# Kernel tuning notes

Hardware: AMD Instinct MI355X
Metric: run time of the kernel (lower is better)

Reference implementation:

```python
import jax, jax.numpy as jnp
import numpy as np

B, S, DIM = 2, 2048, 4096
H, KV, HD = 32, 8, 128
REP = H // KV
SCALE = HD ** -0.5
ROPE_THETA = 10000.0


def setup_inputs() -> dict:
    key = jax.random.key(0)
    ks = jax.random.split(key, 6)
    x = jax.random.normal(ks[0], (B, S, DIM), dtype=jnp.float32)
    # weights stored [in, out]; y = x @ W matches nn.Linear(in,out,bias=False)
    wq = jax.random.normal(ks[1], (DIM, H * HD), dtype=jnp.float32) * (DIM ** -0.5)
    wk = jax.random.normal(ks[2], (DIM, KV * HD), dtype=jnp.float32) * (DIM ** -0.5)
    wv = jax.random.normal(ks[3], (DIM, KV * HD), dtype=jnp.float32) * (DIM ** -0.5)
    wo = jax.random.normal(ks[4], (H * HD, DIM), dtype=jnp.float32) * ((H * HD) ** -0.5)
    # RoPE tables: angle[t, j] = t * theta^(-2j/hd)
    inv_freq = 1.0 / (ROPE_THETA ** (np.arange(0, HD, 2, dtype=np.float32) / HD))
    t = np.arange(S, dtype=np.float32)
    angles = np.outer(t, inv_freq)  # [S, HD/2]
    freqs_cos = jnp.asarray(np.cos(angles), dtype=jnp.float32)
    freqs_sin = jnp.asarray(np.sin(angles), dtype=jnp.float32)
    # causal additive mask
    neg = jnp.finfo(jnp.float32).min
    mask = jnp.where(jnp.tril(jnp.ones((S, S), dtype=bool)), 0.0, neg).astype(jnp.float32)
    positions = jnp.arange(S, dtype=jnp.int64)
    return {"x": x, "wq": wq, "wk": wk, "wv": wv, "wo": wo,
            "freqs_cos": freqs_cos, "freqs_sin": freqs_sin,
            "mask": mask, "positions": positions}


def _rope(t, cos, sin):
    # t: [b, s, h, hd]; cos/sin: [s, hd/2]
    b, s, h, hd = t.shape
    tr = t.reshape(b, s, h, hd // 2, 2)
    tre, tim = tr[..., 0], tr[..., 1]
    c = cos[None, :, None, :]
    sn = sin[None, :, None, :]
    out_re = tre * c - tim * sn
    out_im = tre * sn + tim * c
    return jnp.stack([out_re, out_im], axis=-1).reshape(b, s, h, hd)


def reference(x, wq, wk, wv, wo, freqs_cos, freqs_sin, mask, positions):
    b, s, _ = x.shape
    xq = (x @ wq).reshape(b, s, H, HD)
    xk = (x @ wk).reshape(b, s, KV, HD)
    xv = (x @ wv).reshape(b, s, KV, HD)
    xq = _rope(xq, freqs_cos, freqs_sin)
    xk = _rope(xk, freqs_cos, freqs_sin)
    # GQA without materializing repeated KV: group query heads by kv head
    q = xq.transpose(0, 2, 1, 3).reshape(b, KV, REP, s, HD)  # [b,g,r,s,d]
    k = xk.transpose(0, 2, 1, 3)                              # [b,g,s,d]
    v = xv.transpose(0, 2, 1, 3)                              # [b,g,s,d]
    scores = jnp.einsum('bgrqd,bgkd->bgrqk', q, k) * SCALE
    scores = scores + mask[None, None, None, :, :]
    probs = jax.nn.softmax(scores.astype(jnp.float32), axis=-1).astype(q.dtype)
    out = jnp.einsum('bgrqk,bgkd->bgrqd', probs, v)           # [b,g,r,s,d]
    out = out.reshape(b, H, s, HD).transpose(0, 2, 1, 3).reshape(b, s, H * HD)
    return out @ wo
```

## Files before the change

### kernel.cpp

```cpp
#include <hip/hip_runtime.h>
#include <math.h>

#define B_ 2
#define S_ 2048
#define DIM_ 4096
#define H_ 32
#define KV_ 8
#define HD_ 128
#define SCALE_ 0.08838834764831844f
#define QSCALE_ 0.12751744154254998f

typedef unsigned short u16;
typedef __attribute__((ext_vector_type(8))) short bf16x8;
typedef __attribute__((ext_vector_type(4))) float f32x4;
typedef __attribute__((ext_vector_type(16))) float f32x16;
typedef __attribute__((ext_vector_type(8))) unsigned short u16x8;
typedef __attribute__((ext_vector_type(4))) unsigned short u16x4;

__device__ __forceinline__ u16 f2b(float f) {
  union { float f; unsigned u; } v; v.f = f;
  unsigned r = v.u + 0x7fffu + ((v.u >> 16) & 1u);
  return (u16)(r >> 16);
}
__device__ __forceinline__ float b2f(u16 h) {
  union { unsigned u; float f; } v; v.u = ((unsigned)h) << 16;
  return v.f;
}
__device__ __forceinline__ unsigned cvt_pk_bf16(float lo, float hi) {
  unsigned r;
  asm("v_cvt_pk_bf16_f32 %0, %1, %2" : "=v"(r) : "v"(lo), "v"(hi));
  return r;
}
__device__ __forceinline__ void async_copy16(const void* g, void* l) {
  __builtin_amdgcn_global_load_lds(
      (const __attribute__((address_space(1))) void*)g,
      (__attribute__((address_space(3))) void*)l, 16, 0, 0);
}
__device__ __forceinline__ void bar() {
  asm volatile("s_barrier" ::: "memory");
}

__global__ __launch_bounds__(256) void cvt_bf16(const float* __restrict__ in,
                                                u16* __restrict__ out, int n4) {
  int i = blockIdx.x * 256 + threadIdx.x;
  if (i >= n4) return;
  float4 v = ((const float4*)in)[i];
  u16x4 o; o[0] = f2b(v.x); o[1] = f2b(v.y); o[2] = f2b(v.z); o[3] = f2b(v.w);
  ((u16x4*)out)[i] = o;
}

__global__ __launch_bounds__(256) void transpose_cvt(
    const float* __restrict__ W, u16* __restrict__ WT, int K, int N) {
  __shared__ float Ts[64][65];
  const int tid = threadIdx.x;
  const int n0 = blockIdx.x * 64, k0 = blockIdx.y * 64;
#pragma unroll
  for (int p = 0; p < 4; ++p) {
    int r = p * 16 + (tid >> 4), c = (tid & 15) * 4;
    float4 v = *(const float4*)(W + (size_t)(k0 + r) * N + n0 + c);
    Ts[r][c] = v.x; Ts[r][c + 1] = v.y; Ts[r][c + 2] = v.z; Ts[r][c + 3] = v.w;
  }
  __syncthreads();
#pragma unroll
  for (int p = 0; p < 4; ++p) {
    int n = p * 16 + (tid >> 4), kq = (tid & 15) * 4;
    u16x4 o;
    o[0] = f2b(Ts[kq + 0][n]); o[1] = f2b(Ts[kq + 1][n]);
    o[2] = f2b(Ts[kq + 2][n]); o[3] = f2b(Ts[kq + 3][n]);
    *(u16x4*)(WT + (size_t)(n0 + n) * K + k0 + kq) = o;
  }
}

__global__ __launch_bounds__(256) void rope_bf16(unsigned* __restrict__ T,
                                                 const float* __restrict__ cs,
                                                 const float* __restrict__ sn,
                                                 int total, float scale) {
  int idx = blockIdx.x * 256 + threadIdx.x;
  if (idx >= total) return;
  int i = idx & 63, s = (idx >> 6) & (S_ - 1);
  float c = cs[s * 64 + i], si = sn[s * 64 + i];
  unsigned v = T[idx];
  float re = b2f((u16)(v & 0xffffu)), im = b2f((u16)(v >> 16));
  float ore = (re * c - im * si) * scale, oim = (re * si + im * c) * scale;
  T[idx] = (unsigned)f2b(ore) | ((unsigned)f2b(oim) << 16);
}

__global__ __launch_bounds__(256) void gemm_kv(
    const u16* __restrict__ A, const u16* __restrict__ Bt,
    u16* __restrict__ Kh, u16* __restrict__ Vt, int M, int N, int K) {
  __shared__ u16 As[128 * 64];
  __shared__ u16 Bs[128 * 64];
  const int tid = threadIdx.x, lane = tid & 63;
  const int wbase = tid & ~63;
  const int o = blockIdx.y * gridDim.x + blockIdx.x;
  const int q8 = (gridDim.x * gridDim.y) >> 3;
  const int p = (o & 7) * q8 + (o >> 3);
  const int row0 = (p / gridDim.x) * 128, col0 = (p % gridDim.x) * 128;
  const int wm = ((tid >> 6) >> 1) * 64, wn = ((tid >> 6) & 1) * 64;

  f32x4 acc[4][4];
#pragma unroll
  for (int i = 0; i < 4; ++i)
#pragma unroll
    for (int j = 0; j < 4; ++j) acc[i][j] = (f32x4){0.f, 0.f, 0.f, 0.f};

  const int nk = K >> 6;
  for (int kt = 0; kt < nk; ++kt) {
    const int k0 = kt << 6;
#pragma unroll
    for (int i = 0; i < 4; ++i) {
      int g = i * 256 + tid;
      int r = g >> 3, ss = (g & 7) ^ (r & 7);
      async_copy16(A + (size_t)(row0 + r) * K + k0 + ss * 8,
                   (char*)As + (i * 256 + wbase) * 16);
    }
#pragma unroll
    for (int i = 0; i < 4; ++i) {
      int g = i * 256 + tid;
      int r = g >> 3, ss = (g & 7) ^ (r & 7);
      async_copy16(Bt + (size_t)(col0 + r) * K + k0 + ss * 8,
                   (char*)Bs + (i * 256 + wbase) * 16);
    }
    __syncthreads();
#pragma unroll
    for (int ks = 0; ks < 2; ++ks) {
      bf16x8 af[4], bf[4];
#pragma unroll
      for (int mi = 0; mi < 4; ++mi) {
        int r = wm + mi * 16 + (lane & 15);
        int off = (ks * 64 + ((lane >> 4) << 4)) ^ ((r & 7) << 4);
        af[mi] = *(const bf16x8*)((const char*)As + r * 128 + off);
      }
#pragma unroll
      for (int ni = 0; ni < 4; ++ni) {
        int r = wn + ni * 16 + (lane & 15);
        int off = (ks * 64 + ((lane >> 4) << 4)) ^ ((r & 7) << 4);
        bf[ni] = *(const bf16x8*)((const char*)Bs + r * 128 + off);
      }
#pragma unroll
      for (int mi = 0; mi < 4; ++mi)
#pragma unroll
        for (int ni = 0; ni < 4; ++ni)
          acc[mi][ni] = __builtin_amdgcn_mfma_f32_16x16x32_bf16(
              af[mi], bf[ni], acc[mi][ni], 0, 0, 0);
    }
    __syncthreads();
  }

#pragma unroll
  for (int mi = 0; mi < 4; ++mi)
#pragma unroll
    for (int ni = 0; ni < 4; ++ni) {
      const int mb = row0 + wm + mi * 16 + ((lane >> 4) << 2);
      const int n = col0 + wn + ni * 16 + (lane & 15);
      const int b = mb >> 11, s0 = mb & (S_ - 1);
      const int hh = n >> 7, d = n & (HD_ - 1);
      if (hh < 8) {
#pragma unroll
        for (int r = 0; r < 4; ++r)
          Kh[(((size_t)(b * 8 + hh)) * S_ + s0 + r) * HD_ + d] =
              f2b(acc[mi][ni][r]);
      } else {
        u16x4 ov;
#pragma unroll
        for (int r = 0; r < 4; ++r) ov[r] = f2b(acc[mi][ni][r]);
        *(u16x4*)(Vt + (((size_t)(b * 8 + (hh & 7)) * HD_ + d) * S_ + s0)) = ov;
      }
    }
}

template <int OUT_MODE>
__global__ __launch_bounds__(512) void gemm256(
    const u16* __restrict__ A, const u16* __restrict__ Bt,
    void* __restrict__ Cout, int M, int N, int K, int heads) {
  __shared__ u16 lds[65536];
  char* const ldsb = (char*)lds;
  const int tid = threadIdx.x, lane = tid & 63, wid = tid >> 6;
  const int q = lane & 15, g = lane >> 4;
  const int wm = wid >> 2, wn = wid & 3;
  const int o = blockIdx.y * gridDim.x + blockIdx.x;
  const int q8 = (gridDim.x * gridDim.y) >> 3;
  const int p = (o & 7) * q8 + (o >> 3);
  const int row0 = (p / gridDim.x) * 256, col0 = (p % gridDim.x) * 256;
  const int nk = K >> 6, nh = nk << 2;

  const u16* srcA[2];
  const u16* srcB[2];
#pragma unroll
  for (int u = 0; u < 2; ++u) {
    int j = u * 512 + tid;
    int row = ((j >> 3) << 1) + ((j >> 2) & 1);
    int colg = (j & 3) ^ ((j >> 3) & 3);
    srcA[u] = A + (size_t)(row0 + row) * K + colg * 8;
    srcB[u] = Bt + (size_t)(col0 + row) * K + colg * 8;
  }

  auto STAGE = [&](int h) {
    if (h >= nh) return;
    int tau = h >> 2, ks = (h >> 1) & 1, op = h & 1;
    int slot = (2 * tau + ks) & 3;
    int koff = tau * 64 + ks * 32;
    char* lbase = ldsb + op * 65536 + slot * 16384 + wid * 1024;
#pragma unroll
    for (int u = 0; u < 2; ++u)
      async_copy16((op ? srcB[u] : srcA[u]) + koff, lbase + u * 8192);
  };

  int aread[8], bread[4];
#pragma unroll
  for (int mi = 0; mi < 8; ++mi) {
    int row = wm * 128 + mi * 16 + q;
    aread[mi] = (row >> 1) * 128 + (row & 1) * 64 + ((g ^ ((row >> 1) & 3)) << 4);
  }
#pragma unroll
  for (int ni = 0; ni < 4; ++ni) {
    int row = wn * 64 + ni * 16 + q;
    bread[ni] = (row >> 1) * 128 + (row & 1) * 64 + ((g ^ ((row >> 1) & 3)) << 4);
  }

  f32x4 acc[8][4];
#pragma unroll
  for (int i = 0; i < 8; ++i)
#pragma unroll
    for (int j = 0; j < 4; ++j) acc[i][j] = (f32x4){0.f, 0.f, 0.f, 0.f};

  auto RDA = [&](bf16x8* d, const char* s, int ob) {
#pragma unroll
    for (int i = 0; i < 4; ++i) d[i] = *(const bf16x8*)(s + aread[ob + i]);
  };
  auto RDB = [&](bf16x8* d, const char* s) {
#pragma unroll
    for (int i = 0; i < 4; ++i) d[i] = *(const bf16x8*)(s + bread[i]);
  };
  auto MFMA16 = [&](int mo, bf16x8* af, bf16x8* bfr) {
    __builtin_amdgcn_s_setprio(1);
#pragma unroll
    for (int mi = 0; mi < 4; ++mi)
#pragma unroll
      for (int ni = 0; ni < 4; ++ni)
        acc[mo + mi][ni] = __builtin_amdgcn_mfma_f32_16x16x32_bf16(
            af[mi], bfr[ni], acc[mo + mi][ni], 0, 0, 0);
    __builtin_amdgcn_s_setprio(0);
  };

#pragma unroll
  for (int h = 0; h < 6; ++h) STAGE(h);
  asm volatile("s_waitcnt vmcnt(4)" ::: "memory");
  bar();
  bf16x8 afc[4], afn[4], bfc[4], bfn[4];
  RDA(afc, ldsb, 0);
  RDB(bfc, ldsb + 65536);

  for (int t = 0; t < nk; ++t) {
    const int s0 = (2 * t) & 3, s1 = (2 * t + 1) & 3;
    const char* As0 = ldsb + s0 * 16384;
    const char* Bs1 = ldsb + 65536 + s1 * 16384;
    const char* As1 = ldsb + s1 * 16384;

    STAGE(4 * t + 6);
    bar();
    MFMA16(0, afc, bfc);
    RDA(afn, As0, 4);
    bar();

    STAGE(4 * t + 7);
    bar();
    MFMA16(4, afn, bfc);
    RDA(afc, As1, 0);
    RDB(bfn, Bs1);
    bar();

    STAGE(4 * t + 8);
    bar();
    MFMA16(0, afc, bfn);
    RDA(afn, As1, 4);
    bar();

    STAGE(4 * t + 9);
    bar();
    MFMA16(4, afn, bfn);
    if (t < nk - 2)
      asm volatile("s_waitcnt vmcnt(4)" ::: "memory");
    else if (t == nk - 2)
      asm volatile("s_waitcnt vmcnt(0)" ::: "memory");
    if (t < nk - 1) {
      const char* As0n = ldsb + ((2 * t + 2) & 3) * 16384;
      const char* Bs0n = ldsb + 65536 + ((2 * t + 2) & 3) * 16384;
      RDA(afc, As0n, 0);
      RDB(bfc, Bs0n);
    }
    bar();
  }

#pragma unroll
  for (int mi = 0; mi < 8; ++mi)
#pragma unroll
    for (int ni = 0; ni < 4; ++ni) {
      int mb = row0 + wm * 128 + mi * 16 + (g << 2);
      int n = col0 + wn * 64 + ni * 16 + q;
#pragma unroll
      for (int r = 0; r < 4; ++r) {
        int m = mb + r;
        float v = acc[mi][ni][r];
        if (OUT_MODE == 0) {
          ((float*)Cout)[(size_t)m * N + n] = v;
        } else {
          int b = m >> 11, s = m & (S_ - 1);
          int h = n >> 7, d = n & (HD_ - 1);
          ((u16*)Cout)[(((size_t)(b * heads + h)) * S_ + s) * HD_ + d] = f2b(v);
        }
      }
    }
}

__global__ __launch_bounds__(256, 2) void attn_mfma(
    const u16* __restrict__ Qb, const u16* __restrict__ Kb,
    const u16* __restrict__ Vt, u16* __restrict__ AO,
    const float* __restrict__ fc, const float* __restrict__ fs) {
  __shared__ u16 Ks[2][64 * 128];
  __shared__ u16 Vs[2][128 * 64];

  const int tid = threadIdx.x, lane = tid & 63, wid = tid >> 6;
  const int wbase = tid & ~63;
  const int o = blockIdx.x + (blockIdx.y << 3) + (blockIdx.z << 8);
  const int pid = o >> 6, h = o & 31, b = (o >> 5) & 1;
  const int kvh = h >> 2;
  const int l31 = lane & 31, hi = lane >> 5;

  const u16* Kbase = Kb + ((size_t)(b * KV_ + kvh) * S_) * HD_;
  const u16* Vbase = Vt + ((size_t)(b * KV_ + kvh) * HD_) * S_;

  const u16* Kl[4];
  const u16* Vl[4];
#pragma unroll
  for (int i = 0; i < 4; ++i) {
    int gg = i * 256 + tid;
    int rK = gg >> 4, ssK = (gg & 15) ^ (rK & 7);
    Kl[i] = Kbase + (size_t)rK * HD_ + ssK * 8;
    int rV = gg >> 3, ssV = (gg & 7) ^ (rV & 7);
    Vl[i] = Vbase + (size_t)rV * S_ + ssV * 8;
  }

  auto STAGE_KV = [&](int kt, int buf) {
    const int kv0 = kt * 64;
#pragma unroll
    for (int i = 0; i < 4; ++i)
      async_copy16(Kl[i] + (size_t)kv0 * HD_,
                   (char*)Ks[buf] + (i * 256 + wbase) * 16);
#pragma unroll
    for (int i = 0; i < 4; ++i)
      async_copy16(Vl[i] + kv0, (char*)Vs[buf] + (i * 256 + wbase) * 16);
  };

  for (int half = 0; half < 2; ++half) {
    const int qt = half ? (15 - pid) : pid;
    const int q0 = qt * 128;
    const int qg = q0 + wid * 32 + l31;

    STAGE_KV(0, 0);

    bf16x8 qf[8];
    {
      const u16* qrow = Qb + ((size_t)(b * H_ + h) * S_ + qg) * HD_ + hi * 8;
      const float* cb = fc + qg * 64 + hi * 4;
      const float* sb = fs + qg * 64 + hi * 4;
#pragma unroll
      for (int ks = 0; ks < 8; ++ks) {
        u16x8 v = *(const u16x8*)(qrow + ks * 16);
        float4 cv = *(const float4*)(cb + ks * 8);
        float4 sv = *(const float4*)(sb + ks * 8);
        unsigned w[4];
#pragma unroll
        for (int j = 0; j < 4; ++j) {
          float c = ((const float*)&cv)[j] * QSCALE_;
          float s = ((const float*)&sv)[j] * QSCALE_;
          float re = b2f((u16)v[2 * j]), im = b2f((u16)v[2 * j + 1]);
          w[j] = cvt_pk_bf16(re * c - im * s, re * s + im * c);
        }
        union { unsigned u[4]; bf16x8 q; } cvt;
        cvt.u[0] = w[0]; cvt.u[1] = w[1]; cvt.u[2] = w[2]; cvt.u[3] = w[3];
        qf[ks] = cvt.q;
      }
    }

    f32x16 oacc[4];
#pragma unroll
    for (int i = 0; i < 4; ++i)
#pragma unroll
      for (int j = 0; j < 16; ++j) oacc[i][j] = 0.f;
    float mrow = -3e38f, lrow = 0.f;

    __syncthreads();

    const int nkt = 2 * qt + 2;
    for (int kt = 0; kt < nkt; ++kt) {
      const int cur = kt & 1;
      if (kt + 1 < nkt) STAGE_KV(kt + 1, cur ^ 1);
      const char* Kc = (const char*)Ks[cur];
      const char* Vc = (const char*)Vs[cur];
      const int kv0 = kt * 64;

      f32x16 sacc[2];
#pragma unroll
      for (int kf = 0; kf < 2; ++kf)
#pragma unroll
        for (int j = 0; j < 16; ++j) sacc[kf][j] = 0.f;
      __builtin_amdgcn_s_setprio(1);
#pragma unroll
      for (int ks = 0; ks < 8; ++ks) {
#pragma unroll
        for (int kf = 0; kf < 2; ++kf) {
          const int arow = kf * 32 + l31;
          bf16x8 kfrag = *(const bf16x8*)(
              Kc + arow * 256 + ((((ks * 2 + hi) << 4)) ^ ((arow & 7) << 4)));
          sacc[kf] = __builtin_amdgcn_mfma_f32_32x32x16_bf16(kfrag, qf[ks],
                                                             sacc[kf], 0, 0, 0);
        }
      }
      __builtin_amdgcn_s_setprio(0);

      if (kv0 + 63 > q0 + wid * 32) {
#pragma unroll
        for (int kf = 0; kf < 2; ++kf)
#pragma unroll
          for (int r = 0; r < 16; ++r) {
            int kg = kv0 + kf * 32 + (r & 3) + 8 * (r >> 2) + 4 * hi;
            if (kg > qg) sacc[kf][r] = -3e38f;
          }
      }

      float m0 = -3e38f, m1 = -3e38f, m2 = -3e38f, m3 = -3e38f;
#pragma unroll
      for (int kf = 0; kf < 2; ++kf)
#pragma unroll
        for (int r = 0; r < 4; ++r) {
          m0 = fmaxf(m0, sacc[kf][r]);
          m1 = fmaxf(m1, sacc[kf][r + 4]);
          m2 = fmaxf(m2, sacc[kf][r + 8]);
          m3 = fmaxf(m3, sacc[kf][r + 12]);
        }
      float rmax = fmaxf(fmaxf(m0, m1), fmaxf(m2, m3));
      rmax = fmaxf(rmax, __shfl_xor(rmax, 32, 64));
      const bool defer = __all(rmax - mrow <= 11.5f);
      float mnew, fsc;
      if (defer) {
        mnew = mrow; fsc = 1.0f;
      } else {
        mnew = fmaxf(mrow, rmax); fsc = exp2f(mrow - mnew);
      }
      mrow = mnew;
      float p0 = 0.f, p1 = 0.f, p2 = 0.f, p3 = 0.f;
#pragma unroll
      for (int kf = 0; kf < 2; ++kf)
#pragma unroll
        for (int r = 0; r < 4; ++r) {
          float e0 = exp2f(sacc[kf][r] - mnew);
          float e1 = exp2f(sacc[kf][r + 4] - mnew);
          float e2 = exp2f(sacc[kf][r + 8] - mnew);
          float e3 = exp2f(sacc[kf][r + 12] - mnew);
          sacc[kf][r] = e0; sacc[kf][r + 4] = e1;
          sacc[kf][r + 8] = e2; sacc[kf][r + 12] = e3;
          p0 += e0; p1 += e1; p2 += e2; p3 += e3;
        }
      float psum = (p0 + p1) + (p2 + p3);
      psum += __shfl_xor(psum, 32, 64);
      lrow = lrow * fsc + psum;

      if (!defer) {
#pragma unroll
        for (int r = 0; r < 16; ++r) {
          float fr = __shfl(fsc, (r & 3) + 8 * (r >> 2) + 4 * hi, 64);
#pragma unroll
          for (int df = 0; df < 4; ++df) oacc[df][r] *= fr;
        }
      }

      bf16x8 pa[4];
#pragma unroll
      for (int kf = 0; kf < 2; ++kf) {
        unsigned w0 = cvt_pk_bf16(sacc[kf][0], sacc[kf][1]);
        unsigned w1 = cvt_pk_bf16(sacc[kf][2], sacc[kf][3]);
        unsigned w2 = cvt_pk_bf16(sacc[kf][4], sacc[kf][5]);
        unsigned w3 = cvt_pk_bf16(sacc[kf][6], sacc[kf][7]);
        unsigned w4 = cvt_pk_bf16(sacc[kf][8], sacc[kf][9]);
        unsigned w5 = cvt_pk_bf16(sacc[kf][10], sacc[kf][11]);
        unsigned w6 = cvt_pk_bf16(sacc[kf][12], sacc[kf][13]);
        unsigned w7 = cvt_pk_bf16(sacc[kf][14], sacc[kf][15]);
        asm volatile("v_permlane32_swap_b32 %0, %1" : "+v"(w0), "+v"(w2));
        asm volatile("v_permlane32_swap_b32 %0, %1" : "+v"(w1), "+v"(w3));
        asm volatile("v_permlane32_swap_b32 %0, %1" : "+v"(w4), "+v"(w6));
        asm volatile("v_permlane32_swap_b32 %0, %1" : "+v"(w5), "+v"(w7));
        union { unsigned u[4]; bf16x8 q; } f0, f1;
        f0.u[0] = w0; f0.u[1] = w1; f0.u[2] = w2; f0.u[3] = w3;
        f1.u[0] = w4; f1.u[1] = w5; f1.u[2] = w6; f1.u[3] = w7;
        pa[kf * 2] = f0.q;
        pa[kf * 2 + 1] = f1.q;
      }

      __builtin_amdgcn_s_setprio(1);
#pragma unroll
      for (int ks = 0; ks < 4; ++ks) {
#pragma unroll
        for (int df = 0; df < 4; ++df) {
          const int vrow = df * 32 + l31;
          bf16x8 vf = *(const bf16x8*)(
              Vc + vrow * 128 + ((((ks * 2 + hi) << 4)) ^ ((vrow & 7) << 4)));
          oacc[df] = __builtin_amdgcn_mfma_f32_32x32x16_bf16(pa[ks], vf,
                                                             oacc[df], 0, 0, 0);
        }
      }
      __builtin_amdgcn_s_setprio(0);
      __syncthreads();
    }

    const float linv = 1.f / lrow;
#pragma unroll
    for (int r = 0; r < 16; ++r) {
      const int qloc = (r & 3) + 8 * (r >> 2) + 4 * hi;
      const float invq = __shfl(linv, qloc, 64);
      const int sq = q0 + wid * 32 + qloc;
      u16* dst = AO + (size_t)(b * S_ + sq) * (H_ * HD_) + h * HD_ + l31;
#pragma unroll
      for (int df = 0; df < 4; ++df) dst[df * 32] = f2b(oacc[df][r] * invq);
    }
  }
}

extern "C" void kernel_launch(void* const* d_in, const int* in_sizes, int n_in,
                              void* d_out, int out_size, void* d_ws, size_t ws_size,
                              hipStream_t stream) {
  const float* x  = (const float*)d_in[0];
  const float* wq = (const float*)d_in[1];
  const float* wk = (const float*)d_in[2];
  const float* wv = (const float*)d_in[3];
  const float* wo = (const float*)d_in[4];
  const float* fc = (const float*)d_in[5];
  const float* fs = (const float*)d_in[6];
  float* out = (float*)d_out;

  u16* ws  = (u16*)d_ws;
  u16* wqT = ws;
  u16* VtB = ws;
  u16* xb  = ws + 16777216;
  u16* AOb = xb;
  u16* woT = ws + 33554432;
  u16* Qh  = ws + 50331648;
  u16* wkT = ws + 67108864;
  u16* wvT = ws + 71303168;
  u16* Kh  = ws + 75497472;

  dim3 blk(256);

  cvt_bf16<<<dim3(16384), blk, 0, stream>>>(x, xb, 4194304);
  transpose_cvt<<<dim3(64, 64), blk, 0, stream>>>(wq, wqT, DIM_, H_ * HD_);
  transpose_cvt<<<dim3(16, 64), blk, 0, stream>>>(wk, wkT, DIM_, KV_ * HD_);
  transpose_cvt<<<dim3(16, 64), blk, 0, stream>>>(wv, wvT, DIM_, KV_ * HD_);
  transpose_cvt<<<dim3(64, 64), blk, 0, stream>>>(wo, woT, H_ * HD_, DIM_);

  gemm256<1><<<dim3(16, 16), dim3(512), 0, stream>>>(xb, wqT, Qh, 4096, 4096, 4096, H_);
  gemm_kv<<<dim3(16, 32), blk, 0, stream>>>(xb, wkT, Kh, VtB, 4096, 2048, 4096);

  rope_bf16<<<dim3(8192), blk, 0, stream>>>((unsigned*)Kh, fc, fs, 2097152, 1.0f);

  attn_mfma<<<dim3(8, 32, 2), blk, 0, stream>>>(Qh, Kh, VtB, AOb, fc, fs);

  gemm256<0><<<dim3(16, 16), dim3(512), 0, stream>>>(AOb, woT, out, 4096, 4096, 4096, 0);
}
```

Baseline: 522.3 us.

## Fuse prep kernels, make GEMM K constexpr, unroll k-loop, drop attention setprio

Merges the x conversion and the four weight transpose-convert launches into one kernel that dispatches on block index, removing four launches and the gaps between them. The 256-tile GEMM gets a compile-time K and a 2x-unrolled main loop. The s_setprio hints around the attention MFMA blocks are removed. These are unrelated tweaks. The larger fused prep kernel may carry register/LDS cost in the x-path blocks, and the unroll may raise register pressure.

```diff
diff --git a/kernel.cpp b/kernel.cpp
--- a/kernel.cpp
+++ b/kernel.cpp
@@ -40,25 +40,36 @@
   asm volatile("s_barrier" ::: "memory");
 }
 
-__global__ __launch_bounds__(256) void cvt_bf16(const float* __restrict__ in,
-                                                u16* __restrict__ out, int n4) {
-  int i = blockIdx.x * 256 + threadIdx.x;
-  if (i >= n4) return;
-  float4 v = ((const float4*)in)[i];
-  u16x4 o; o[0] = f2b(v.x); o[1] = f2b(v.y); o[2] = f2b(v.z); o[3] = f2b(v.w);
-  ((u16x4*)out)[i] = o;
-}
-
-__global__ __launch_bounds__(256) void transpose_cvt(
-    const float* __restrict__ W, u16* __restrict__ WT, int K, int N) {
+__global__ __launch_bounds__(256) void prep_fused(
+    const float* __restrict__ x, u16* __restrict__ xb,
+    const float* __restrict__ wq, u16* __restrict__ wqT,
+    const float* __restrict__ wk, u16* __restrict__ wkT,
+    const float* __restrict__ wv, u16* __restrict__ wvT,
+    const float* __restrict__ wo, u16* __restrict__ woT) {
   __shared__ float Ts[64][65];
   const int tid = threadIdx.x;
-  const int n0 = blockIdx.x * 64, k0 = blockIdx.y * 64;
+  const int bid = blockIdx.x;
+
+  if (bid < 16384) {
+    int i = bid * 256 + tid;
+    float4 v = ((const float4*)x)[i];
+    u16x4 o; o[0] = f2b(v.x); o[1] = f2b(v.y); o[2] = f2b(v.z); o[3] = f2b(v.w);
+    ((u16x4*)xb)[i] = o;
+    return;
+  }
+
+  const float* W; u16* WT; int K, N, gx, v;
+  if (bid < 20480)      { W = wq; WT = wqT; K = DIM_; N = H_ * HD_;  gx = 64; v = bid - 16384; }
+  else if (bid < 21504) { W = wk; WT = wkT; K = DIM_; N = KV_ * HD_; gx = 16; v = bid - 20480; }
+  else if (bid < 22528) { W = wv; WT = wvT; K = DIM_; N = KV_ * HD_; gx = 16; v = bid - 21504; }
+  else                  { W = wo; WT = woT; K = H_ * HD_; N = DIM_;  gx = 64; v = bid - 22528; }
+  const int n0 = (v % gx) * 64, k0 = (v / gx) * 64;
+
 #pragma unroll
   for (int p = 0; p < 4; ++p) {
     int r = p * 16 + (tid >> 4), c = (tid & 15) * 4;
-    float4 v = *(const float4*)(W + (size_t)(k0 + r) * N + n0 + c);
-    Ts[r][c] = v.x; Ts[r][c + 1] = v.y; Ts[r][c + 2] = v.z; Ts[r][c + 3] = v.w;
+    float4 w = *(const float4*)(W + (size_t)(k0 + r) * N + n0 + c);
+    Ts[r][c] = w.x; Ts[r][c + 1] = w.y; Ts[r][c + 2] = w.z; Ts[r][c + 3] = w.w;
   }
   __syncthreads();
 #pragma unroll
@@ -172,7 +183,10 @@
 template <int OUT_MODE>
 __global__ __launch_bounds__(512) void gemm256(
     const u16* __restrict__ A, const u16* __restrict__ Bt,
-    void* __restrict__ Cout, int M, int N, int K, int heads) {
+    void* __restrict__ Cout, int M, int N, int heads) {
+  constexpr int K = 4096;
+  constexpr int nk = K >> 6;
+  constexpr int nh = nk << 2;
   __shared__ u16 lds[65536];
   char* const ldsb = (char*)lds;
   const int tid = threadIdx.x, lane = tid & 63, wid = tid >> 6;
@@ -182,7 +196,6 @@
   const int q8 = (gridDim.x * gridDim.y) >> 3;
   const int p = (o & 7) * q8 + (o >> 3);
   const int row0 = (p / gridDim.x) * 256, col0 = (p % gridDim.x) * 256;
-  const int nk = K >> 6, nh = nk << 2;
 
   const u16* srcA[2];
   const u16* srcB[2];
@@ -251,6 +264,7 @@
   RDA(afc, ldsb, 0);
   RDB(bfc, ldsb + 65536);
 
+#pragma unroll 2
   for (int t = 0; t < nk; ++t) {
     const int s0 = (2 * t) & 3, s1 = (2 * t + 1) & 3;
     const char* As0 = ldsb + s0 * 16384;
@@ -405,7 +419,6 @@
       for (int kf = 0; kf < 2; ++kf)
 #pragma unroll
         for (int j = 0; j < 16; ++j) sacc[kf][j] = 0.f;
-      __builtin_amdgcn_s_setprio(1);
 #pragma unroll
       for (int ks = 0; ks < 8; ++ks) {
 #pragma unroll
@@ -417,7 +430,6 @@
                                                              sacc[kf], 0, 0, 0);
         }
       }
-      __builtin_amdgcn_s_setprio(0);
 
       if (kv0 + 63 > q0 + wid * 32) {
 #pragma unroll
@@ -497,7 +509,6 @@
         pa[kf * 2 + 1] = f1.q;
       }
 
-      __builtin_amdgcn_s_setprio(1);
 #pragma unroll
       for (int ks = 0; ks < 4; ++ks) {
 #pragma unroll
@@ -509,7 +520,6 @@
                                                              oacc[df], 0, 0, 0);
         }
       }
-      __builtin_amdgcn_s_setprio(0);
       __syncthreads();
     }
 
@@ -551,18 +561,15 @@
 
   dim3 blk(256);
 
-  cvt_bf16<<<dim3(16384), blk, 0, stream>>>(x, xb, 4194304);
-  transpose_cvt<<<dim3(64, 64), blk, 0, stream>>>(wq, wqT, DIM_, H_ * HD_);
-  transpose_cvt<<<dim3(16, 64), blk, 0, stream>>>(wk, wkT, DIM_, KV_ * HD_);
-  transpose_cvt<<<dim3(16, 64), blk, 0, stream>>>(wv, wvT, DIM_, KV_ * HD_);
-  transpose_cvt<<<dim3(64, 64), blk, 0, stream>>>(wo, woT, H_ * HD_, DIM_);
-
-  gemm256<1><<<dim3(16, 16), dim3(512), 0, stream>>>(xb, wqT, Qh, 4096, 4096, 4096, H_);
+  prep_fused<<<dim3(26624), blk, 0, stream>>>(x, xb, wq, wqT, wk, wkT, wv, wvT,
+                                              wo, woT);
+
+  gemm256<1><<<dim3(16, 16), dim3(512), 0, stream>>>(xb, wqT, Qh, 4096, 4096, H_);
   gemm_kv<<<dim3(16, 32), blk, 0, stream>>>(xb, wkT, Kh, VtB, 4096, 2048, 4096);
 
   rope_bf16<<<dim3(8192), blk, 0, stream>>>((unsigned*)Kh, fc, fs, 2097152, 1.0f);
 
   attn_mfma<<<dim3(8, 32, 2), blk, 0, stream>>>(Qh, Kh, VtB, AOb, fc, fs);
 
-  gemm256<0><<<dim3(16, 16), dim3(512), 0, stream>>>(AOb, woT, out, 4096, 4096, 4096, 0);
-}
+  gemm256<0><<<dim3(16, 16), dim3(512), 0, stream>>>(AOb, woT, out, 4096, 4096, 0);
+}
```

Result: faster. 508.5 us (-2.6%).
